# Performance work log

Measured on AMD Instinct MI355X. Metric: run time of the kernel, lower is better.

The kernel has to match this reference:

```python
import jax, jax.numpy as jnp
import numpy as np

B, L, D, U = 4, 1024, 64, 32

def setup_inputs() -> dict:
    key = jax.random.key(0)
    ks = jax.random.split(key, 6)
    inputs = jax.random.normal(ks[0], (B, L, D), dtype=jnp.float32)
    Wt = jax.random.normal(ks[1], (D, U), dtype=jnp.float32) * 0.1
    Wx = jax.random.normal(ks[2], (D, U), dtype=jnp.float32) * 0.1
    Wa = jax.random.normal(ks[3], (U, 1), dtype=jnp.float32) * 0.1
    bh = jax.random.normal(ks[4], (U,), dtype=jnp.float32) * 0.1
    ba = jax.random.normal(ks[5], (1,), dtype=jnp.float32) * 0.1
    return {"inputs": inputs, "Wt": Wt, "Wx": Wx, "Wa": Wa,
            "bh": bh, "ba": ba, "attention_width": 0}

def reference(inputs, Wt, Wx, Wa, bh, ba, attention_width):
    # Additive (Bahdanau) self-attention emission.
    q = inputs @ Wt                              # (B, L, U)
    k = inputs @ Wx                              # (B, L, U)
    # broadcast add -> (B, L, L, U), the dominant intermediate
    h = jnp.tanh(q[:, :, None, :] + k[:, None, :, :] + bh)
    e = jnp.squeeze(h @ Wa, axis=-1) + ba        # (B, L, L); ba broadcasts
    # NOTE: attention_width mask is dead code in the original forward -> ignored.
    # manual max-subtracted softmax with +1e-8 denominator (as in source)
    m = jnp.max(e, axis=-1, keepdims=True)
    ex = jnp.exp(e - m)
    a = ex / (jnp.sum(ex, axis=-1, keepdims=True) + 1e-8)
    v = jnp.einsum('bij,bjd->bid', a, inputs)    # (B, L, D)
    return v
```

## Files before the change

kernel.cpp:

```cpp
#include <hip/hip_runtime.h>

#define BB 4
#define LL 1024
#define DD 64
#define UU 32
#define TI 8
#define NT 512
#define JH 512

__global__ __launch_bounds__(256) void precompute_kernel(
    const float* __restrict__ inp, const float* __restrict__ Wx,
    float* __restrict__ Ekt)
{
    __shared__ float s_in[8][DD];
    __shared__ float s_wx[DD][UU];
    __shared__ float s_ek[8][36];
    int t = threadIdx.x;
    int row0 = blockIdx.x * 8;
    if (t < 128)
        ((float4*)s_in)[t] = ((const float4*)(inp + (size_t)row0 * DD))[t];
#pragma unroll
    for (int p = 0; p < 2; ++p)
        ((float4*)s_wx)[p * 256 + t] = ((const float4*)Wx)[p * 256 + t];
    __syncthreads();
    int r = t >> 5;
    int u = t & 31;
    float k = 0.f;
#pragma unroll
    for (int d = 0; d < DD; ++d)
        k = fmaf(s_in[r][d], s_wx[d][u], k);
    s_ek[r][u] = __expf(2.f * k);
    __syncthreads();
    if (t < 64) {
        int u4 = t >> 3, r2 = t & 7;
        float4 v = *(const float4*)(&s_ek[r2][u4 * 4]);
        size_t gr = row0 + r2;
        size_t bb_ = gr >> 10, l = gr & 1023;
        ((float4*)Ekt)[(bb_ * 8 + u4) * LL + l] = v;
    }
}

union ShMem {
    struct { float wt[DD][UU]; float in[TI][DD]; } pre;
    struct { float a[JH][TI]; } sm;
    float4 v[8][TI][16];
};

__global__ __launch_bounds__(NT) void attn_partial_kernel(
    const float* __restrict__ Ekt, const float* __restrict__ inp,
    const float* __restrict__ Wt, const float* __restrict__ Wa,
    const float* __restrict__ bh,
    float* __restrict__ po, float* __restrict__ pm, float* __restrict__ ps)
{
    __shared__ ShMem sh;
    __shared__ float s_eq[TI][UU];
    __shared__ float s_red[2][8][TI];

    int t      = threadIdx.x;
    int w      = t >> 6;
    int bid    = blockIdx.x;
    int rowblk = bid >> 1;
    int jh     = bid & 1;
    int b      = rowblk >> 7;
    int i0     = (rowblk & 127) * TI;
    int j0     = jh * JH;

    if (t < 128)
        ((float4*)sh.pre.in)[t] =
            ((const float4*)(inp + (size_t)(b * LL + i0) * DD))[t];
    ((float4*)sh.pre.wt)[t] = ((const float4*)Wt)[t];
    __syncthreads();
    if (t < TI * UU) {
        int i = t >> 5, u = t & 31;
        float q = 0.f;
#pragma unroll
        for (int d = 0; d < DD; ++d)
            q = fmaf(sh.pre.in[i][d], sh.pre.wt[d][u], q);
        s_eq[i][u] = __expf(2.f * (q + bh[u]));
    }
    __syncthreads();

    const float4* ektb = (const float4*)Ekt + (size_t)b * 8 * LL;
    float acc[TI];
#pragma unroll
    for (int i = 0; i < TI; ++i) acc[i] = 0.f;

    float4 cur = ektb[j0 + t];

#pragma unroll
    for (int u4 = 0; u4 < 8; ++u4) {
        float4 nxt;
        if (u4 < 7) nxt = ektb[(u4 + 1) * LL + j0 + t];
        float4 wav = *(const float4*)(Wa + u4 * 4);
        float wa0 = wav.x, wa1 = wav.y, wa2 = wav.z, wa3 = wav.w;
#pragma unroll
        for (int i = 0; i < TI; ++i) {
            float4 eqv = *(const float4*)(&s_eq[i][u4 * 4]);
            float p  = fmaf(eqv.x, cur.x, 1.f);
            float q  = fmaf(eqv.y, cur.y, 1.f);
            float r  = fmaf(eqv.z, cur.z, 1.f);
            float s  = fmaf(eqv.w, cur.w, 1.f);
            float n01 = fmaf(wa0, q, wa1 * p);
            float n23 = fmaf(wa2, s, wa3 * r);
            float pq = p * q, rs = r * s;
            float num = fmaf(n01, rs, n23 * pq);
            float den = pq * rs;
            acc[i] = fmaf(num, __builtin_amdgcn_rcpf(den), acc[i]);
        }
        if (u4 < 7) cur = nxt;
    }

    float ev[TI];
#pragma unroll
    for (int i = 0; i < TI; ++i) ev[i] = -2.f * acc[i];

    float wred[TI];
#pragma unroll
    for (int i = 0; i < TI; ++i) {
        float v = ev[i];
#pragma unroll
        for (int m = 32; m >= 1; m >>= 1) v = fmaxf(v, __shfl_xor(v, m, 64));
        wred[i] = v;
    }
    if ((t & 63) == 0) {
#pragma unroll
        for (int i = 0; i < TI; ++i) s_red[0][w][i] = wred[i];
    }
    __syncthreads();
    float m[TI];
#pragma unroll
    for (int i = 0; i < TI; ++i) {
        float v = s_red[0][0][i];
#pragma unroll
        for (int w2 = 1; w2 < 8; ++w2) v = fmaxf(v, s_red[0][w2][i]);
        m[i] = v;
    }

#pragma unroll
    for (int i = 0; i < TI; ++i) {
        ev[i] = __expf(ev[i] - m[i]);
        float s = ev[i];
#pragma unroll
        for (int mm = 32; mm >= 1; mm >>= 1) s += __shfl_xor(s, mm, 64);
        wred[i] = s;
    }
    if ((t & 63) == 0) {
#pragma unroll
        for (int i = 0; i < TI; ++i) s_red[1][w][i] = wred[i];
    }
    __syncthreads();
    float sl[TI];
#pragma unroll
    for (int i = 0; i < TI; ++i) {
        float s = 0.f;
#pragma unroll
        for (int w2 = 0; w2 < 8; ++w2) s += s_red[1][w2][i];
        sl[i] = s;
    }
    if (t == 0) {
#pragma unroll
        for (int i = 0; i < TI; ++i) {
            pm[rowblk * 16 + jh * 8 + i] = m[i];
            ps[rowblk * 16 + jh * 8 + i] = sl[i];
        }
    }

    {
        float4 lo, hi;
        lo.x = ev[0]; lo.y = ev[1]; lo.z = ev[2]; lo.w = ev[3];
        hi.x = ev[4]; hi.y = ev[5]; hi.z = ev[6]; hi.w = ev[7];
        *(float4*)(&sh.sm.a[t][0]) = lo;
        *(float4*)(&sh.sm.a[t][4]) = hi;
    }
    __syncthreads();

    int dq = t & 15;
    int g  = t >> 4;
    const float4* inp4 = (const float4*)(inp + (size_t)b * LL * DD);
    float4 v[TI];
#pragma unroll
    for (int i = 0; i < TI; ++i) v[i] = (float4){0.f, 0.f, 0.f, 0.f};

#pragma unroll 4
    for (int jj = 0; jj < 16; ++jj) {
        int jl = jj * 32 + g;
        float4 x  = inp4[(size_t)(j0 + jl) * 16 + dq];
        float4 a0 = *(const float4*)(&sh.sm.a[jl][0]);
        float4 a1 = *(const float4*)(&sh.sm.a[jl][4]);
        v[0].x = fmaf(a0.x, x.x, v[0].x); v[0].y = fmaf(a0.x, x.y, v[0].y);
        v[0].z = fmaf(a0.x, x.z, v[0].z); v[0].w = fmaf(a0.x, x.w, v[0].w);
        v[1].x = fmaf(a0.y, x.x, v[1].x); v[1].y = fmaf(a0.y, x.y, v[1].y);
        v[1].z = fmaf(a0.y, x.z, v[1].z); v[1].w = fmaf(a0.y, x.w, v[1].w);
        v[2].x = fmaf(a0.z, x.x, v[2].x); v[2].y = fmaf(a0.z, x.y, v[2].y);
        v[2].z = fmaf(a0.z, x.z, v[2].z); v[2].w = fmaf(a0.z, x.w, v[2].w);
        v[3].x = fmaf(a0.w, x.x, v[3].x); v[3].y = fmaf(a0.w, x.y, v[3].y);
        v[3].z = fmaf(a0.w, x.z, v[3].z); v[3].w = fmaf(a0.w, x.w, v[3].w);
        v[4].x = fmaf(a1.x, x.x, v[4].x); v[4].y = fmaf(a1.x, x.y, v[4].y);
        v[4].z = fmaf(a1.x, x.z, v[4].z); v[4].w = fmaf(a1.x, x.w, v[4].w);
        v[5].x = fmaf(a1.y, x.x, v[5].x); v[5].y = fmaf(a1.y, x.y, v[5].y);
        v[5].z = fmaf(a1.y, x.z, v[5].z); v[5].w = fmaf(a1.y, x.w, v[5].w);
        v[6].x = fmaf(a1.z, x.x, v[6].x); v[6].y = fmaf(a1.z, x.y, v[6].y);
        v[6].z = fmaf(a1.z, x.z, v[6].z); v[6].w = fmaf(a1.z, x.w, v[6].w);
        v[7].x = fmaf(a1.w, x.x, v[7].x); v[7].y = fmaf(a1.w, x.y, v[7].y);
        v[7].z = fmaf(a1.w, x.z, v[7].z); v[7].w = fmaf(a1.w, x.w, v[7].w);
    }

#pragma unroll
    for (int i = 0; i < TI; ++i) {
        v[i].x += __shfl_xor(v[i].x, 16, 64); v[i].y += __shfl_xor(v[i].y, 16, 64);
        v[i].z += __shfl_xor(v[i].z, 16, 64); v[i].w += __shfl_xor(v[i].w, 16, 64);
        v[i].x += __shfl_xor(v[i].x, 32, 64); v[i].y += __shfl_xor(v[i].y, 32, 64);
        v[i].z += __shfl_xor(v[i].z, 32, 64); v[i].w += __shfl_xor(v[i].w, 32, 64);
    }
    __syncthreads();
    if ((t & 63) < 16) {
#pragma unroll
        for (int i = 0; i < TI; ++i) sh.v[w][i][dq] = v[i];
    }
    __syncthreads();

    int i = t >> 6;
    int d = t & 63;
    const float* svf = (const float*)sh.v;
    float r = 0.f;
#pragma unroll
    for (int w2 = 0; w2 < 8; ++w2) r += svf[w2 * (TI * 64) + i * 64 + d];
    po[(size_t)bid * (TI * DD) + i * DD + d] = r;
}

__global__ __launch_bounds__(256) void combine_kernel(
    const float* __restrict__ po, const float* __restrict__ pm,
    const float* __restrict__ ps, float* __restrict__ out)
{
    int gid    = blockIdx.x * 256 + threadIdx.x;
    int d      = gid & 63;
    int row    = gid >> 6;
    int rowblk = row >> 3;
    int i      = row & 7;
    float m0 = pm[rowblk * 16 + i],     m1 = pm[rowblk * 16 + 8 + i];
    float s0 = ps[rowblk * 16 + i],     s1 = ps[rowblk * 16 + 8 + i];
    float m  = fmaxf(m0, m1);
    float w0 = __expf(m0 - m), w1 = __expf(m1 - m);
    float s  = fmaf(s0, w0, s1 * w1) + 1e-8f;
    float o0 = po[(size_t)(rowblk * 2 + 0) * 512 + i * 64 + d];
    float o1 = po[(size_t)(rowblk * 2 + 1) * 512 + i * 64 + d];
    out[(size_t)row * DD + d] = fmaf(o0, w0, o1 * w1) * __builtin_amdgcn_rcpf(s);
}

extern "C" void kernel_launch(void* const* d_in, const int* in_sizes, int n_in,
                              void* d_out, int out_size, void* d_ws, size_t ws_size,
                              hipStream_t stream) {
    const float* inp = (const float*)d_in[0];
    const float* Wt  = (const float*)d_in[1];
    const float* Wx  = (const float*)d_in[2];
    const float* Wa  = (const float*)d_in[3];
    const float* bh  = (const float*)d_in[4];
    float* out = (float*)d_out;

    float* Ekt = (float*)d_ws;
    float* po  = Ekt + (size_t)BB * LL * UU;
    float* pm  = po + (size_t)1024 * TI * DD;
    float* ps  = pm + (size_t)512 * 16;

    precompute_kernel<<<BB * LL / 8, 256, 0, stream>>>(inp, Wx, Ekt);
    attn_partial_kernel<<<2 * BB * LL / TI, NT, 0, stream>>>(
        Ekt, inp, Wt, Wa, bh, po, pm, ps);
    combine_kernel<<<BB * LL * DD / 256, 256, 0, stream>>>(po, pm, ps, out);
}
```

Baseline: 104.0 us.

## Remap attention blocks to one query row per wavefront with scalar-broadcast query terms

```diff
diff --git a/kernel.cpp b/kernel.cpp
--- a/kernel.cpp
+++ b/kernel.cpp
@@ -4,9 +4,10 @@
 #define LL 1024
 #define DD 64
 #define UU 32
-#define TI 8
-#define NT 512
+#define NW 4
+#define NT 256
 #define JH 512
+#define NTILE 8
 
 __global__ __launch_bounds__(256) void precompute_kernel(
     const float* __restrict__ inp, const float* __restrict__ Wx,
@@ -40,210 +41,161 @@
     }
 }
 
-union ShMem {
-    struct { float wt[DD][UU]; float in[TI][DD]; } pre;
-    struct { float a[JH][TI]; } sm;
-    float4 v[8][TI][16];
-};
-
 __global__ __launch_bounds__(NT) void attn_partial_kernel(
     const float* __restrict__ Ekt, const float* __restrict__ inp,
     const float* __restrict__ Wt, const float* __restrict__ Wa,
     const float* __restrict__ bh,
     float* __restrict__ po, float* __restrict__ pm, float* __restrict__ ps)
 {
-    __shared__ ShMem sh;
-    __shared__ float s_eq[TI][UU];
-    __shared__ float s_red[2][8][TI];
-
-    int t      = threadIdx.x;
-    int w      = t >> 6;
-    int bid    = blockIdx.x;
-    int rowblk = bid >> 1;
-    int jh     = bid & 1;
-    int b      = rowblk >> 7;
-    int i0     = (rowblk & 127) * TI;
-    int j0     = jh * JH;
-
-    if (t < 128)
+    __shared__ union {
+        struct { float wt[DD][UU]; float in[NW][DD]; } pre;
+        float a[NW][JH];
+    } sh;
+    __shared__ float  s_eq[NW][UU];
+    __shared__ float4 s_v[NW][NW][16];
+
+    int t    = threadIdx.x;
+    int w    = t >> 6;
+    int lane = t & 63;
+    int bid  = blockIdx.x;
+    int q    = bid >> 1;
+    int h    = bid & 1;
+    int b    = q >> 8;
+    int i0   = (q & 255) * NW;
+    int j0   = h * JH;
+
+    if (t < 64)
         ((float4*)sh.pre.in)[t] =
             ((const float4*)(inp + (size_t)(b * LL + i0) * DD))[t];
-    ((float4*)sh.pre.wt)[t] = ((const float4*)Wt)[t];
-    __syncthreads();
-    if (t < TI * UU) {
-        int i = t >> 5, u = t & 31;
-        float q = 0.f;
+    ((float4*)sh.pre.wt)[t]       = ((const float4*)Wt)[t];
+    ((float4*)sh.pre.wt)[t + 256] = ((const float4*)Wt)[t + 256];
+    __syncthreads();
+    if (t < NW * UU) {
+        int r = t >> 5, u = t & 31;
+        float qq = 0.f;
 #pragma unroll
         for (int d = 0; d < DD; ++d)
-            q = fmaf(sh.pre.in[i][d], sh.pre.wt[d][u], q);
-        s_eq[i][u] = __expf(2.f * (q + bh[u]));
-    }
-    __syncthreads();
+            qq = fmaf(sh.pre.in[r][d], sh.pre.wt[d][u], qq);
+        s_eq[r][u] = __expf(2.f * (qq + bh[u]));
+    }
+    __syncthreads();
+
+    float eqv = s_eq[w][lane & 31];
+    float sq[UU];
+#pragma unroll
+    for (int u = 0; u < UU; ++u)
+        sq[u] = __uint_as_float(
+            __builtin_amdgcn_readlane(__float_as_uint(eqv), u));
 
     const float4* ektb = (const float4*)Ekt + (size_t)b * 8 * LL;
-    float acc[TI];
-#pragma unroll
-    for (int i = 0; i < TI; ++i) acc[i] = 0.f;
-
-    float4 cur = ektb[j0 + t];
-
-#pragma unroll
-    for (int u4 = 0; u4 < 8; ++u4) {
-        float4 nxt;
-        if (u4 < 7) nxt = ektb[(u4 + 1) * LL + j0 + t];
-        float4 wav = *(const float4*)(Wa + u4 * 4);
-        float wa0 = wav.x, wa1 = wav.y, wa2 = wav.z, wa3 = wav.w;
-#pragma unroll
-        for (int i = 0; i < TI; ++i) {
-            float4 eqv = *(const float4*)(&s_eq[i][u4 * 4]);
-            float p  = fmaf(eqv.x, cur.x, 1.f);
-            float q  = fmaf(eqv.y, cur.y, 1.f);
-            float r  = fmaf(eqv.z, cur.z, 1.f);
-            float s  = fmaf(eqv.w, cur.w, 1.f);
-            float n01 = fmaf(wa0, q, wa1 * p);
-            float n23 = fmaf(wa2, s, wa3 * r);
-            float pq = p * q, rs = r * s;
+    float rmax = -3.4e38f;
+#pragma unroll 2
+    for (int tile = 0; tile < NTILE; ++tile) {
+        int jj = j0 + tile * 64 + lane;
+        float4 ek[8];
+#pragma unroll
+        for (int u4 = 0; u4 < 8; ++u4) ek[u4] = ektb[u4 * LL + jj];
+        float acc = 0.f;
+#pragma unroll
+        for (int u4 = 0; u4 < 8; ++u4) {
+            float4 wav = *(const float4*)(Wa + u4 * 4);
+            float p  = fmaf(sq[u4 * 4 + 0], ek[u4].x, 1.f);
+            float qq = fmaf(sq[u4 * 4 + 1], ek[u4].y, 1.f);
+            float r  = fmaf(sq[u4 * 4 + 2], ek[u4].z, 1.f);
+            float s  = fmaf(sq[u4 * 4 + 3], ek[u4].w, 1.f);
+            float n01 = fmaf(wav.x, qq, wav.y * p);
+            float n23 = fmaf(wav.z, s, wav.w * r);
+            float pq = p * qq, rs = r * s;
             float num = fmaf(n01, rs, n23 * pq);
-            float den = pq * rs;
-            acc[i] = fmaf(num, __builtin_amdgcn_rcpf(den), acc[i]);
+            acc = fmaf(num, __builtin_amdgcn_rcpf(pq * rs), acc);
         }
-        if (u4 < 7) cur = nxt;
-    }
-
-    float ev[TI];
-#pragma unroll
-    for (int i = 0; i < TI; ++i) ev[i] = -2.f * acc[i];
-
-    float wred[TI];
-#pragma unroll
-    for (int i = 0; i < TI; ++i) {
-        float v = ev[i];
-#pragma unroll
-        for (int m = 32; m >= 1; m >>= 1) v = fmaxf(v, __shfl_xor(v, m, 64));
-        wred[i] = v;
-    }
-    if ((t & 63) == 0) {
-#pragma unroll
-        for (int i = 0; i < TI; ++i) s_red[0][w][i] = wred[i];
-    }
-    __syncthreads();
-    float m[TI];
-#pragma unroll
-    for (int i = 0; i < TI; ++i) {
-        float v = s_red[0][0][i];
-#pragma unroll
-        for (int w2 = 1; w2 < 8; ++w2) v = fmaxf(v, s_red[0][w2][i]);
-        m[i] = v;
-    }
-
-#pragma unroll
-    for (int i = 0; i < TI; ++i) {
-        ev[i] = __expf(ev[i] - m[i]);
-        float s = ev[i];
-#pragma unroll
-        for (int mm = 32; mm >= 1; mm >>= 1) s += __shfl_xor(s, mm, 64);
-        wred[i] = s;
-    }
-    if ((t & 63) == 0) {
-#pragma unroll
-        for (int i = 0; i < TI; ++i) s_red[1][w][i] = wred[i];
-    }
-    __syncthreads();
-    float sl[TI];
-#pragma unroll
-    for (int i = 0; i < TI; ++i) {
-        float s = 0.f;
-#pragma unroll
-        for (int w2 = 0; w2 < 8; ++w2) s += s_red[1][w2][i];
-        sl[i] = s;
-    }
-    if (t == 0) {
-#pragma unroll
-        for (int i = 0; i < TI; ++i) {
-            pm[rowblk * 16 + jh * 8 + i] = m[i];
-            ps[rowblk * 16 + jh * 8 + i] = sl[i];
-        }
-    }
-
-    {
-        float4 lo, hi;
-        lo.x = ev[0]; lo.y = ev[1]; lo.z = ev[2]; lo.w = ev[3];
-        hi.x = ev[4]; hi.y = ev[5]; hi.z = ev[6]; hi.w = ev[7];
-        *(float4*)(&sh.sm.a[t][0]) = lo;
-        *(float4*)(&sh.sm.a[t][4]) = hi;
+        float e = -2.f * acc;
+        rmax = fmaxf(rmax, e);
+        sh.a[w][tile * 64 + lane] = e;
+    }
+
+#pragma unroll
+    for (int m2 = 32; m2 >= 1; m2 >>= 1)
+        rmax = fmaxf(rmax, __shfl_xor(rmax, m2, 64));
+    float sum = 0.f;
+#pragma unroll
+    for (int tile = 0; tile < NTILE; ++tile) {
+        float e  = sh.a[w][tile * 64 + lane];
+        float ex = __expf(e - rmax);
+        sum += ex;
+        sh.a[w][tile * 64 + lane] = ex;
+    }
+#pragma unroll
+    for (int m2 = 32; m2 >= 1; m2 >>= 1)
+        sum += __shfl_xor(sum, m2, 64);
+    if (lane == 0) {
+        pm[bid * NW + w] = rmax;
+        ps[bid * NW + w] = sum;
     }
     __syncthreads();
 
     int dq = t & 15;
     int g  = t >> 4;
     const float4* inp4 = (const float4*)(inp + (size_t)b * LL * DD);
-    float4 v[TI];
-#pragma unroll
-    for (int i = 0; i < TI; ++i) v[i] = (float4){0.f, 0.f, 0.f, 0.f};
+    float4 v[NW];
+#pragma unroll
+    for (int i = 0; i < NW; ++i) v[i] = (float4){0.f, 0.f, 0.f, 0.f};
 
 #pragma unroll 4
-    for (int jj = 0; jj < 16; ++jj) {
-        int jl = jj * 32 + g;
+    for (int jj = 0; jj < JH / 16; ++jj) {
+        int jl = jj * 16 + g;
         float4 x  = inp4[(size_t)(j0 + jl) * 16 + dq];
-        float4 a0 = *(const float4*)(&sh.sm.a[jl][0]);
-        float4 a1 = *(const float4*)(&sh.sm.a[jl][4]);
-        v[0].x = fmaf(a0.x, x.x, v[0].x); v[0].y = fmaf(a0.x, x.y, v[0].y);
-        v[0].z = fmaf(a0.x, x.z, v[0].z); v[0].w = fmaf(a0.x, x.w, v[0].w);
-        v[1].x = fmaf(a0.y, x.x, v[1].x); v[1].y = fmaf(a0.y, x.y, v[1].y);
-        v[1].z = fmaf(a0.y, x.z, v[1].z); v[1].w = fmaf(a0.y, x.w, v[1].w);
-        v[2].x = fmaf(a0.z, x.x, v[2].x); v[2].y = fmaf(a0.z, x.y, v[2].y);
-        v[2].z = fmaf(a0.z, x.z, v[2].z); v[2].w = fmaf(a0.z, x.w, v[2].w);
-        v[3].x = fmaf(a0.w, x.x, v[3].x); v[3].y = fmaf(a0.w, x.y, v[3].y);
-        v[3].z = fmaf(a0.w, x.z, v[3].z); v[3].w = fmaf(a0.w, x.w, v[3].w);
-        v[4].x = fmaf(a1.x, x.x, v[4].x); v[4].y = fmaf(a1.x, x.y, v[4].y);
-        v[4].z = fmaf(a1.x, x.z, v[4].z); v[4].w = fmaf(a1.x, x.w, v[4].w);
-        v[5].x = fmaf(a1.y, x.x, v[5].x); v[5].y = fmaf(a1.y, x.y, v[5].y);
-        v[5].z = fmaf(a1.y, x.z, v[5].z); v[5].w = fmaf(a1.y, x.w, v[5].w);
-        v[6].x = fmaf(a1.z, x.x, v[6].x); v[6].y = fmaf(a1.z, x.y, v[6].y);
-        v[6].z = fmaf(a1.z, x.z, v[6].z); v[6].w = fmaf(a1.z, x.w, v[6].w);
-        v[7].x = fmaf(a1.w, x.x, v[7].x); v[7].y = fmaf(a1.w, x.y, v[7].y);
-        v[7].z = fmaf(a1.w, x.z, v[7].z); v[7].w = fmaf(a1.w, x.w, v[7].w);
-    }
-
-#pragma unroll
-    for (int i = 0; i < TI; ++i) {
+        float a0 = sh.a[0][jl], a1 = sh.a[1][jl];
+        float a2 = sh.a[2][jl], a3 = sh.a[3][jl];
+        v[0].x = fmaf(a0, x.x, v[0].x); v[0].y = fmaf(a0, x.y, v[0].y);
+        v[0].z = fmaf(a0, x.z, v[0].z); v[0].w = fmaf(a0, x.w, v[0].w);
+        v[1].x = fmaf(a1, x.x, v[1].x); v[1].y = fmaf(a1, x.y, v[1].y);
+        v[1].z = fmaf(a1, x.z, v[1].z); v[1].w = fmaf(a1, x.w, v[1].w);
+        v[2].x = fmaf(a2, x.x, v[2].x); v[2].y = fmaf(a2, x.y, v[2].y);
+        v[2].z = fmaf(a2, x.z, v[2].z); v[2].w = fmaf(a2, x.w, v[2].w);
+        v[3].x = fmaf(a3, x.x, v[3].x); v[3].y = fmaf(a3, x.y, v[3].y);
+        v[3].z = fmaf(a3, x.z, v[3].z); v[3].w = fmaf(a3, x.w, v[3].w);
+    }
+
+#pragma unroll
+    for (int i = 0; i < NW; ++i) {
         v[i].x += __shfl_xor(v[i].x, 16, 64); v[i].y += __shfl_xor(v[i].y, 16, 64);
         v[i].z += __shfl_xor(v[i].z, 16, 64); v[i].w += __shfl_xor(v[i].w, 16, 64);
         v[i].x += __shfl_xor(v[i].x, 32, 64); v[i].y += __shfl_xor(v[i].y, 32, 64);
         v[i].z += __shfl_xor(v[i].z, 32, 64); v[i].w += __shfl_xor(v[i].w, 32, 64);
     }
-    __syncthreads();
-    if ((t & 63) < 16) {
-#pragma unroll
-        for (int i = 0; i < TI; ++i) sh.v[w][i][dq] = v[i];
+    if (lane < 16) {
+#pragma unroll
+        for (int i = 0; i < NW; ++i) s_v[w][i][dq] = v[i];
     }
     __syncthreads();
 
     int i = t >> 6;
     int d = t & 63;
-    const float* svf = (const float*)sh.v;
+    const float* svf = (const float*)s_v;
     float r = 0.f;
 #pragma unroll
-    for (int w2 = 0; w2 < 8; ++w2) r += svf[w2 * (TI * 64) + i * 64 + d];
-    po[(size_t)bid * (TI * DD) + i * DD + d] = r;
+    for (int w2 = 0; w2 < NW; ++w2) r += svf[w2 * (NW * 64) + i * 64 + d];
+    po[(size_t)bid * (NW * DD) + i * DD + d] = r;
 }
 
 __global__ __launch_bounds__(256) void combine_kernel(
     const float* __restrict__ po, const float* __restrict__ pm,
     const float* __restrict__ ps, float* __restrict__ out)
 {
-    int gid    = blockIdx.x * 256 + threadIdx.x;
-    int d      = gid & 63;
-    int row    = gid >> 6;
-    int rowblk = row >> 3;
-    int i      = row & 7;
-    float m0 = pm[rowblk * 16 + i],     m1 = pm[rowblk * 16 + 8 + i];
-    float s0 = ps[rowblk * 16 + i],     s1 = ps[rowblk * 16 + 8 + i];
+    int gid = blockIdx.x * 256 + threadIdx.x;
+    int d   = gid & 63;
+    int row = gid >> 6;
+    int q   = row >> 2;
+    int i   = row & 3;
+    int b0  = q * 2, b1 = q * 2 + 1;
+    float m0 = pm[b0 * NW + i], m1 = pm[b1 * NW + i];
+    float s0 = ps[b0 * NW + i], s1 = ps[b1 * NW + i];
     float m  = fmaxf(m0, m1);
     float w0 = __expf(m0 - m), w1 = __expf(m1 - m);
     float s  = fmaf(s0, w0, s1 * w1) + 1e-8f;
-    float o0 = po[(size_t)(rowblk * 2 + 0) * 512 + i * 64 + d];
-    float o1 = po[(size_t)(rowblk * 2 + 1) * 512 + i * 64 + d];
+    float o0 = po[(size_t)b0 * (NW * DD) + i * DD + d];
+    float o1 = po[(size_t)b1 * (NW * DD) + i * DD + d];
     out[(size_t)row * DD + d] = fmaf(o0, w0, o1 * w1) * __builtin_amdgcn_rcpf(s);
 }
 
@@ -259,11 +211,11 @@
 
     float* Ekt = (float*)d_ws;
     float* po  = Ekt + (size_t)BB * LL * UU;
-    float* pm  = po + (size_t)1024 * TI * DD;
-    float* ps  = pm + (size_t)512 * 16;
+    float* pm  = po + (size_t)2048 * NW * DD;
+    float* ps  = pm + (size_t)2048 * NW;
 
     precompute_kernel<<<BB * LL / 8, 256, 0, stream>>>(inp, Wx, Ekt);
-    attn_partial_kernel<<<2 * BB * LL / TI, NT, 0, stream>>>(
+    attn_partial_kernel<<<2 * BB * LL / NW, NT, 0, stream>>>(
         Ekt, inp, Wt, Wa, bh, po, pm, ps);
     combine_kernel<<<BB * LL * DD / 256, 256, 0, stream>>>(po, pm, ps, out);
 }
```

Result: faster. 99.71 us (-4.1%).
